# Kernel optimization log

Hardware: AMD Instinct MI355X
Metric: run time of the kernel (lower is better)

## Reference

```python
import jax, jax.numpy as jnp
import numpy as np

T, NNODES, DEG = 32, 10000, 32
IN_DIM, H1, HEADS, H2, GRU, PH = 128, 32, 4, 32, 32, 5


def setup_inputs() -> dict:
    key = jax.random.key(0)
    ks = jax.random.split(key, 24)
    d = {}
    d["h"] = jax.random.normal(ks[0], (T, NNODES, IN_DIM), jnp.float32)
    d["src"] = jax.random.randint(ks[1], (NNODES, DEG), 0, NNODES, dtype=jnp.int32)
    d["N"] = jnp.ones((1,), jnp.float32)
    d["I"] = jax.random.uniform(ks[2], (T,), jnp.float32)
    d["R"] = jax.random.uniform(ks[3], (T,), jnp.float32)
    d["S"] = jax.random.uniform(ks[4], (T,), jnp.float32)
    d["It"] = jax.random.uniform(ks[5], (T,), jnp.float32)
    d["Rt"] = jax.random.uniform(ks[6], (T,), jnp.float32)
    d["hx0"] = jax.random.normal(ks[7], (1, GRU), jnp.float32)
    # layer1: HEADS independent GATLayers (fc no-bias, attn_fc no-bias)
    d["W1"] = jax.random.normal(ks[8], (HEADS, IN_DIM, H1), jnp.float32) / np.sqrt(IN_DIM)
    d["a1"] = jax.random.normal(ks[9], (HEADS, 2 * H1), jnp.float32) / np.sqrt(2 * H1)
    # layer2: single head over concatenated features
    d["W2"] = jax.random.normal(ks[10], (1, HEADS * H1, H2), jnp.float32) / np.sqrt(HEADS * H1)
    d["a2"] = jax.random.normal(ks[11], (1, 2 * H2), jnp.float32) / np.sqrt(2 * H2)
    # GRUCell params (torch layout: W_ih [3*gru, in], W_hh [3*gru, gru])
    sg = 1.0 / np.sqrt(GRU)
    d["W_ih"] = jax.random.normal(ks[12], (3 * GRU, H2), jnp.float32) * sg
    d["W_hh"] = jax.random.normal(ks[13], (3 * GRU, GRU), jnp.float32) * sg
    d["b_ih"] = jax.random.normal(ks[14], (3 * GRU,), jnp.float32) * sg
    d["b_hh"] = jax.random.normal(ks[15], (3 * GRU,), jnp.float32) * sg
    sr = 1.0 / np.sqrt(GRU + 2)
    d["Wr1"] = jax.random.normal(ks[16], (2 * PH, GRU + 2), jnp.float32) * sr
    d["br1"] = jax.random.normal(ks[17], (2 * PH,), jnp.float32) * sr
    d["Wr2"] = jax.random.normal(ks[18], (2, GRU + 2), jnp.float32) * sr
    d["br2"] = jax.random.normal(ks[19], (2,), jnp.float32) * sr
    return d


def _gat(x, W, a, src):
    # x: [n, din]; W: [H, din, dout]; a: [H, 2*dout]; src: [n, D] in-neighbor ids
    dout = W.shape[-1]
    z = jnp.einsum('nd,hde->hne', x, W)                    # [H, n, dout]
    zs = z[:, src]                                          # [H, n, D, dout] mailbox of src feats
    e = (jnp.einsum('hnde,he->hnd', zs, a[:, :dout])        # a . z_src part
         + jnp.einsum('hne,he->hn', z, a[:, dout:])[:, :, None])  # a . z_dst part
    alpha = jax.nn.softmax(jax.nn.leaky_relu(e, 0.01), axis=-1)   # softmax over mailbox dim
    return jnp.einsum('hnd,hnde->hne', alpha, zs)           # [H, n, dout]


def reference(h, src, N, I, R, S, It, Rt, hx0, W1, a1, W2, a2,
              W_ih, W_hh, b_ih, b_hh, Wr1, br1, Wr2, br2):
    n = h.shape[1]
    Ns = N.squeeze()

    def step(hx, xs):
        iz, I_t, R_t, S_t, It_t, Rt_t = xs
        h1 = jax.nn.relu(_gat(iz, W1, a1, src))             # [H, n, H1]
        h1 = jnp.transpose(h1, (1, 0, 2)).reshape(n, -1)    # cat heads -> [n, H*H1]
        h2 = _gat(h1, W2, a2, src)[0]                       # [n, H2]
        cur = jnp.max(jax.nn.relu(h2), axis=0)[None, :]     # [1, H2]
        # GRUCell
        gi = cur @ W_ih.T + b_ih
        gh = hx @ W_hh.T + b_hh
        gir, giz, gin = jnp.split(gi, 3, axis=1)
        ghr, ghz, ghn = jnp.split(gh, 3, axis=1)
        r = jax.nn.sigmoid(gir + ghr)
        zg = jax.nn.sigmoid(giz + ghz)
        ng = jnp.tanh(gin + r * ghn)
        hx_new = (1.0 - zg) * ng + zg * hx                  # [1, GRU]
        new_hx = jnp.concatenate([hx_new, It_t.reshape(1, 1), Rt_t.reshape(1, 1)], axis=1)
        pred = (new_hx @ Wr1.T + br1).squeeze()             # [2*PH]
        ab = (new_hx @ Wr2.T + br2).squeeze()               # [2]
        a_s = jax.nn.sigmoid(ab[0])
        b_s = jax.nn.sigmoid(ab[1])
        new_I_t = pred[0::2]
        new_R_t = pred[1::2]
        # SIR physics rollout with detached recurrence
        last_I, last_R, last_S = I_t, R_t, S_t
        phyI, phyR = [], []
        dI = jnp.zeros(())
        dR = jnp.zeros(())
        for i in range(PH):
            if i > 0:
                last_I = last_I + jax.lax.stop_gradient(dI)
                last_R = last_R + jax.lax.stop_gradient(dR)
                last_S = Ns - last_I - last_R
            dI = a_s * last_I * (last_S / Ns) - b_s * last_I
            dR = b_s * last_I
            phyI.append(dI)
            phyR.append(dR)
        return hx_new, (new_I_t, new_R_t, jnp.stack(phyI), jnp.stack(phyR))

    _, (nI, nR, pI, pR) = jax.lax.scan(step, hx0, (h, I, R, S, It, Rt))
    return nI, nR, pI.reshape(-1), pR.reshape(-1)
```

## Files before the change

### kernel.cpp

```cpp
#include <hip/hip_runtime.h>

typedef __attribute__((ext_vector_type(8))) short short8;
typedef __attribute__((ext_vector_type(4))) float floatx4;
typedef __attribute__((ext_vector_type(2))) float float2v;
typedef __attribute__((ext_vector_type(4))) unsigned int uint4v;
typedef __attribute__((ext_vector_type(4))) int int4v;
typedef __attribute__((ext_vector_type(2))) unsigned int uint2v;

__device__ __forceinline__ float bf2f(unsigned short u) {
    return __uint_as_float(((unsigned int)u) << 16);
}
__device__ __forceinline__ unsigned short f2bf(float f) {
    unsigned int x = __float_as_uint(f);
    unsigned int r = (x + 0x7FFFu + ((x >> 16) & 1u)) >> 16;
    return (unsigned short)r;
}
__device__ __forceinline__ float ldf(const void* p, long i, bool f32) {
    return f32 ? ((const float*)p)[i] : bf2f(((const unsigned short*)p)[i]);
}
__device__ __forceinline__ bool detect_f32(const unsigned short* Nv) {
    return Nv[0] == 0;
}

#define P_WIH 0
#define P_WHH 3072
#define P_BIH 6144
#define P_BHH 6240
#define P_WR1 6336
#define P_BR1 6676
#define P_WR2 6686
#define P_BR2 6754
#define P_I   6756
#define P_R   6788
#define P_S   6820
#define P_IT  6852
#define P_RT  6884
#define P_N   6916
#define P_HX0 6917
#define P_TOT 6949

__global__ __launch_bounds__(256) void norm_params(
    const void* W1, const void* a1, const void* W2, const void* a2,
    const void* W_ih, const void* W_hh, const void* b_ih, const void* b_hh,
    const void* Wr1, const void* br1, const void* Wr2, const void* br2,
    const void* Iv, const void* Rv, const void* Sv, const void* Itv, const void* Rtv,
    const void* Nv, const void* hx0,
    float* __restrict__ P, unsigned short* __restrict__ WbT1,
    unsigned short* __restrict__ WbT2)
{
    bool f32 = detect_f32((const unsigned short*)Nv);
    int tid = threadIdx.x;
    struct Item { const void* p; int n; int off; };
    const Item items[15] = {
        {W_ih, 3072, P_WIH}, {W_hh, 3072, P_WHH}, {b_ih, 96, P_BIH}, {b_hh, 96, P_BHH},
        {Wr1, 340, P_WR1}, {br1, 10, P_BR1}, {Wr2, 68, P_WR2}, {br2, 2, P_BR2},
        {Iv, 32, P_I}, {Rv, 32, P_R}, {Sv, 32, P_S}, {Itv, 32, P_IT}, {Rtv, 32, P_RT},
        {Nv, 1, P_N}, {hx0, 32, P_HX0}
    };
    for (int it = 0; it < 15; it++)
        for (int i = tid; i < items[it].n; i += 256)
            P[items[it].off + i] = ldf(items[it].p, i, f32);

    for (int idx = tid; idx < 144 * 128; idx += 256) {
        int col = idx >> 7, k = idx & 127;
        float v = 0.f;
        if (col < 128) {
            int h = col >> 5, e = col & 31;
            v = ldf(W1, (h * 128 + k) * 32 + e, f32);
        } else if (col < 136) {
            int q = col - 128;
            int h = (q < 4) ? q : q - 4;
            int off = (q < 4) ? 0 : 32;
            float s = 0.f;
            for (int e = 0; e < 32; e++)
                s += ldf(W1, (h * 128 + k) * 32 + e, f32) * ldf(a1, h * 64 + off + e, f32);
            v = s;
        }
        WbT1[col * 128 + k] = f2bf(v);
    }
    for (int idx = tid; idx < 48 * 128; idx += 256) {
        int col = idx >> 7, k = idx & 127;
        float v = 0.f;
        if (col < 32) {
            v = ldf(W2, k * 32 + col, f32);
        } else if (col < 34) {
            int off = (col == 32) ? 0 : 32;
            float s = 0.f;
            for (int e = 0; e < 32; e++)
                s += ldf(W2, k * 32 + e, f32) * ldf(a2, off + e, f32);
            v = s;
        }
        WbT2[col * 128 + k] = f2bf(v);
    }
}

template<int NT, int HC, bool DYN>
__global__ __launch_bounds__(256) void gat_linear(
    const void* __restrict__ Xv, const unsigned short* __restrict__ WbT,
    unsigned short* __restrict__ Z, float* __restrict__ EL, float* __restrict__ ER,
    const unsigned short* __restrict__ Nv, long row0)
{
    constexpr int NCOL = NT * 16;
    constexpr int LDW  = 136;
    __shared__ unsigned short Ws[NCOL * LDW];
    int tid = threadIdx.x;
    for (int idx = tid; idx < NCOL * 16; idx += 256) {
        int col = idx >> 4, ch = idx & 15;
        *(uint4v*)(&Ws[col * LDW + ch * 8]) = *(const uint4v*)(&WbT[col * 128 + ch * 8]);
    }
    __syncthreads();

    bool f32 = DYN ? detect_f32(Nv) : false;
    int wave = tid >> 6, lane = tid & 63;
    int l15 = lane & 15, quad = lane >> 4;
    long lrow = (long)blockIdx.x * 64 + wave * 16;

    floatx4 acc[NT];
    floatx4 zz = {0.f, 0.f, 0.f, 0.f};
    #pragma unroll
    for (int i = 0; i < NT; i++) acc[i] = zz;

    long xoff = (row0 + lrow + l15) * 128 + quad * 8;
    #pragma unroll
    for (int kt = 0; kt < 4; kt++) {
        short8 afrag;
        if (DYN && f32) {
            const float* xr = (const float*)Xv + xoff + kt * 32;
            float4 u0 = ((const float4*)xr)[0];
            float4 u1 = ((const float4*)xr)[1];
            union { short8 v; unsigned short u[8]; } af;
            af.u[0] = f2bf(u0.x); af.u[1] = f2bf(u0.y);
            af.u[2] = f2bf(u0.z); af.u[3] = f2bf(u0.w);
            af.u[4] = f2bf(u1.x); af.u[5] = f2bf(u1.y);
            af.u[6] = f2bf(u1.z); af.u[7] = f2bf(u1.w);
            afrag = af.v;
        } else {
            afrag = *(const short8*)((const unsigned short*)Xv + xoff + kt * 32);
        }
        #pragma unroll
        for (int nt = 0; nt < NT; nt++) {
            short8 bfrag = *(const short8*)(&Ws[(nt * 16 + l15) * LDW + kt * 32 + quad * 8]);
            acc[nt] = __builtin_amdgcn_mfma_f32_16x16x32_bf16(afrag, bfrag, acc[nt], 0, 0, 0);
        }
    }

    #pragma unroll
    for (int nt = 0; nt < NT; nt++) {
        int col = nt * 16 + l15;
        #pragma unroll
        for (int r = 0; r < 4; r++) {
            long grow = lrow + quad * 4 + r;
            float v = acc[nt][r];
            if (col < HC * 32) {
                Z[grow * (HC * 32) + col] = f2bf(v);
            } else if (col < HC * 32 + HC) {
                EL[grow * HC + (col - HC * 32)] = v;
            } else if (col < HC * 32 + 2 * HC) {
                ER[grow * HC + (col - HC * 32 - HC)] = v;
            }
        }
    }
}

__global__ __launch_bounds__(256, 4) void gat1_aggr(
    const int* __restrict__ src,
    const unsigned short* __restrict__ Z,
    const float* __restrict__ EL,
    const float* __restrict__ ER,
    unsigned short* __restrict__ H1,
    int NX)
{
    __shared__ float als[4][4][33];
    int tid = threadIdx.x;
    int w = tid >> 6, lane = tid & 63;
    int d31 = lane & 31, g = lane >> 5;
    int fl = lane & 15, q = lane >> 4;
    int h = fl >> 2;

    int bid = blockIdx.x;
    int xcd = bid % NX;
    int j   = bid / NX;
    int tq  = j / 2500;
    int r   = j - tq * 2500;
    int t   = tq * NX + xcd;
    int tb  = t * 10000;
    int n   = r * 4 + w;
    int u   = tb + n;
    const char* Zb = (const char*)Z + (size_t)tb * 256;

    int sidx = src[n * 32 + d31];
    float2v el = *(const float2v*)(EL + (size_t)(tb + sidx) * 4 + g * 2);
    float2v er = *(const float2v*)(ER + (size_t)u * 4 + g * 2);
    float e0 = el[0] + er[0], e1 = el[1] + er[1];
    e0 = e0 >= 0.f ? e0 : 0.01f * e0;
    e1 = e1 >= 0.f ? e1 : 0.01f * e1;
    float m0 = e0, m1 = e1;
    #pragma unroll
    for (int off = 16; off > 0; off >>= 1) {
        m0 = fmaxf(m0, __shfl_xor(m0, off));
        m1 = fmaxf(m1, __shfl_xor(m1, off));
    }
    float x0 = __expf(e0 - m0), x1 = __expf(e1 - m1);
    float s0 = x0, s1 = x1;
    #pragma unroll
    for (int off = 16; off > 0; off >>= 1) {
        s0 += __shfl_xor(s0, off);
        s1 += __shfl_xor(s1, off);
    }
    als[w][2 * g + 0][d31] = x0 / s0;
    als[w][2 * g + 1][d31] = x1 / s1;
    __builtin_amdgcn_wave_barrier();

    const int* srow = src + n * 32 + q * 8;
    int4v mma = *(const int4v*)srow;
    int4v mmb = *(const int4v*)(srow + 4);

    uint4v ld[8];
    #pragma unroll
    for (int jj = 0; jj < 8; jj++) {
        int mm = (jj < 4) ? mma[jj & 3] : mmb[jj & 3];
        ld[jj] = *(const uint4v*)(Zb + (unsigned int)(mm * 256 + fl * 16));
    }
    float av[8];
    #pragma unroll
    for (int jj = 0; jj < 8; jj++)
        av[jj] = als[w][h][q * 8 + jj];

    float2v c[4];
    #pragma unroll
    for (int i = 0; i < 4; i++) c[i] = (float2v){0.f, 0.f};
    #pragma unroll
    for (int jj = 0; jj < 8; jj++) {
        float2v a2 = {av[jj], av[jj]};
        float2v f0 = {__uint_as_float(ld[jj].x << 16), __uint_as_float(ld[jj].x & 0xffff0000u)};
        float2v f1 = {__uint_as_float(ld[jj].y << 16), __uint_as_float(ld[jj].y & 0xffff0000u)};
        float2v f2 = {__uint_as_float(ld[jj].z << 16), __uint_as_float(ld[jj].z & 0xffff0000u)};
        float2v f3 = {__uint_as_float(ld[jj].w << 16), __uint_as_float(ld[jj].w & 0xffff0000u)};
        c[0] += a2 * f0;
        c[1] += a2 * f1;
        c[2] += a2 * f2;
        c[3] += a2 * f3;
    }
    #pragma unroll
    for (int i = 0; i < 4; i++) {
        c[i][0] += __shfl_xor(c[i][0], 16);
        c[i][1] += __shfl_xor(c[i][1], 16);
        c[i][0] += __shfl_xor(c[i][0], 32);
        c[i][1] += __shfl_xor(c[i][1], 32);
    }
    if (q == 0) {
        uint4v o;
        #pragma unroll
        for (int i = 0; i < 4; i++) {
            float lo = fmaxf(c[i][0], 0.f);
            float hi = fmaxf(c[i][1], 0.f);
            o[i] = (unsigned int)f2bf(lo) | ((unsigned int)f2bf(hi) << 16);
        }
        __builtin_nontemporal_store(o, (uint4v*)((char*)H1 + (size_t)u * 256 + fl * 16));
    }
}

__global__ __launch_bounds__(256, 4) void gat2_aggr(
    const int* __restrict__ src,
    const unsigned short* __restrict__ Z2,
    const float* __restrict__ EL2,
    const float* __restrict__ ER2,
    int* __restrict__ cur, int t0, int NX)
{
    __shared__ float als2[4][8][32];
    __shared__ int bm[32];
    int tid = threadIdx.x, w = tid >> 6, lane = tid & 63;
    int d31 = lane & 31, g = lane >> 5;
    int g3 = lane >> 3, f7 = lane & 7;

    int bid = blockIdx.x;
    int xcd = bid % NX;
    int j   = bid / NX;
    int tq  = j / 157;
    int r   = j - tq * 157;
    int t   = tq * NX + xcd;
    int tb  = t * 10000;
    int n0  = r * 64 + w * 16;
    const char* Zb = (const char*)Z2 + (size_t)tb * 64;

    if (tid < 32) bm[tid] = 0;
    __syncthreads();

    float m4[4] = {0.f, 0.f, 0.f, 0.f};
    #pragma unroll
    for (int b = 0; b < 2; b++) {
        int nb = n0 + b * 8;
        float ev[8];
        #pragma unroll
        for (int jj = 0; jj < 8; jj++) {
            int n = nb + jj;
            bool ok = n < 10000;
            int sidx = ok ? src[n * 32 + d31] : 0;
            float e = ok ? (EL2[tb + sidx] + ER2[tb + n]) : 0.f;
            ev[jj] = e >= 0.f ? e : 0.01f * e;
        }
        float mx[8];
        #pragma unroll
        for (int jj = 0; jj < 8; jj++) mx[jj] = ev[jj];
        #pragma unroll
        for (int off = 16; off > 0; off >>= 1) {
            #pragma unroll
            for (int jj = 0; jj < 8; jj++)
                mx[jj] = fmaxf(mx[jj], __shfl_xor(mx[jj], off));
        }
        float xv[8], sm[8];
        #pragma unroll
        for (int jj = 0; jj < 8; jj++) { xv[jj] = __expf(ev[jj] - mx[jj]); sm[jj] = xv[jj]; }
        #pragma unroll
        for (int off = 16; off > 0; off >>= 1) {
            #pragma unroll
            for (int jj = 0; jj < 8; jj++)
                sm[jj] += __shfl_xor(sm[jj], off);
        }
        if (g == 0) {
            #pragma unroll
            for (int jj = 0; jj < 8; jj++)
                als2[w][jj][d31] = xv[jj] / sm[jj];
        }
        __builtin_amdgcn_wave_barrier();

        #pragma unroll
        for (int jj = 0; jj < 8; jj++) {
            int n = nb + jj;
            if (n >= 10000) continue;
            floatx4 av4 = *(const floatx4*)&als2[w][jj][g3 * 4];
            int4v mv = *(const int4v*)(src + n * 32 + g3 * 4);
            uint2v ldv[4];
            #pragma unroll
            for (int k = 0; k < 4; k++)
                ldv[k] = *(const uint2v*)(Zb + (unsigned int)(mv[k] * 64 + f7 * 8));
            float c0 = 0.f, c1 = 0.f, c2 = 0.f, c3 = 0.f;
            #pragma unroll
            for (int k = 0; k < 4; k++) {
                c0 += av4[k] * __uint_as_float(ldv[k].x << 16);
                c1 += av4[k] * __uint_as_float(ldv[k].x & 0xffff0000u);
                c2 += av4[k] * __uint_as_float(ldv[k].y << 16);
                c3 += av4[k] * __uint_as_float(ldv[k].y & 0xffff0000u);
            }
            #pragma unroll
            for (int off = 8; off <= 32; off <<= 1) {
                c0 += __shfl_xor(c0, off);
                c1 += __shfl_xor(c1, off);
                c2 += __shfl_xor(c2, off);
                c3 += __shfl_xor(c3, off);
            }
            m4[0] = fmaxf(m4[0], c0);
            m4[1] = fmaxf(m4[1], c1);
            m4[2] = fmaxf(m4[2], c2);
            m4[3] = fmaxf(m4[3], c3);
        }
        __builtin_amdgcn_wave_barrier();
    }
    if (lane < 8) {
        #pragma unroll
        for (int i = 0; i < 4; i++)
            atomicMax(&bm[f7 * 4 + i], __float_as_int(m4[i]));
    }
    __syncthreads();
    if (tid < 32) atomicMax(&cur[(t0 + t) * 32 + tid], bm[tid]);
}

__global__ __launch_bounds__(128) void gru_head(
    const float* __restrict__ P, const float* __restrict__ cur,
    void* __restrict__ outv, const unsigned short* __restrict__ Nv)
{
    bool f32 = detect_f32(Nv);
    __shared__ float Whh[96 * 32], giAll[32 * 96];
    __shared__ float hx[32], gh[96], nh[34];
    int tid = threadIdx.x;
    for (int i = tid; i < 96 * 32; i += 128)
        Whh[i] = P[P_WHH + i];
    for (int o = tid; o < 32 * 96; o += 128) {
        int t = o / 96, gg = o - t * 96;
        float s = P[P_BIH + gg];
        for (int k = 0; k < 32; k++)
            s += cur[t * 32 + k] * P[P_WIH + gg * 32 + k];
        giAll[o] = s;
    }
    if (tid < 32) hx[tid] = P[P_HX0 + tid];
    __syncthreads();

    for (int t = 0; t < 32; t++) {
        if (tid < 96) {
            float sh = 0.f;
            for (int k = 0; k < 32; k++)
                sh += hx[k] * Whh[tid * 32 + k];
            gh[tid] = sh + P[P_BHH + tid];
        }
        __syncthreads();
        if (tid < 32) {
            const float* gi = &giAll[t * 96];
            float r  = 1.f / (1.f + __expf(-(gi[tid] + gh[tid])));
            float zg = 1.f / (1.f + __expf(-(gi[32 + tid] + gh[32 + tid])));
            float ng = tanhf(gi[64 + tid] + r * gh[64 + tid]);
            float hv = (1.f - zg) * ng + zg * hx[tid];
            hx[tid] = hv;
            nh[tid] = hv;
            if (tid == 0) { nh[32] = P[P_IT + t]; nh[33] = P[P_RT + t]; }
        }
        __syncthreads();
        if (tid < 10) {
            float s = P[P_BR1 + tid];
            for (int k = 0; k < 34; k++) s += nh[k] * P[P_WR1 + tid * 34 + k];
            int i = tid >> 1;
            int oi = ((tid & 1) == 0) ? (t * 5 + i) : (160 + t * 5 + i);
            if (f32) ((float*)outv)[oi] = s;
            else     ((unsigned short*)outv)[oi] = f2bf(s);
        }
        if (tid == 64) {
            float ab0 = P[P_BR2 + 0], ab1 = P[P_BR2 + 1];
            for (int k = 0; k < 34; k++) {
                ab0 += nh[k] * P[P_WR2 + k];
                ab1 += nh[k] * P[P_WR2 + 34 + k];
            }
            float a_s = 1.f / (1.f + __expf(-ab0));
            float b_s = 1.f / (1.f + __expf(-ab1));
            float Ns = P[P_N];
            float lI = P[P_I + t], lR = P[P_R + t], lS = P[P_S + t];
            float dI = 0.f, dR = 0.f;
            for (int i = 0; i < 5; i++) {
                if (i > 0) { lI += dI; lR += dR; lS = Ns - lI - lR; }
                dI = a_s * lI * (lS / Ns) - b_s * lI;
                dR = b_s * lI;
                if (f32) {
                    ((float*)outv)[320 + t * 5 + i] = dI;
                    ((float*)outv)[480 + t * 5 + i] = dR;
                } else {
                    ((unsigned short*)outv)[320 + t * 5 + i] = f2bf(dI);
                    ((unsigned short*)outv)[480 + t * 5 + i] = f2bf(dR);
                }
            }
        }
        __syncthreads();
    }
}

extern "C" void kernel_launch(void* const* d_in, const int* in_sizes, int n_in,
                              void* d_out, int out_size, void* d_ws, size_t ws_size,
                              hipStream_t stream) {
    const void* h    = d_in[0];
    const int*  src  = (const int*)d_in[1];
    const void* Nv   = d_in[2];
    const void* Iv   = d_in[3];
    const void* Rv   = d_in[4];
    const void* Sv   = d_in[5];
    const void* Itv  = d_in[6];
    const void* Rtv  = d_in[7];
    const void* hx0  = d_in[8];
    const void* W1   = d_in[9];
    const void* a1   = d_in[10];
    const void* W2   = d_in[11];
    const void* a2   = d_in[12];
    const void* W_ih = d_in[13];
    const void* W_hh = d_in[14];
    const void* b_ih = d_in[15];
    const void* b_hh = d_in[16];
    const void* Wr1  = d_in[17];
    const void* br1  = d_in[18];
    const void* Wr2  = d_in[19];
    const void* br2  = d_in[20];
    const unsigned short* Nu = (const unsigned short*)Nv;

    int TC = 4;
    for (int c = 32; c >= 4; c >>= 1) {
        size_t need = (size_t)c * 10000 * (128 * 2 + 128 * 2 + 16 + 16) + (1 << 20);
        if (need <= ws_size) { TC = c; break; }
    }
    long CR = (long)TC * 10000;

    char* ws = (char*)d_ws;
    size_t off = 0;
    auto alloc = [&](size_t b) {
        void* p = ws + off;
        off += (b + 255) & ~(size_t)255;
        return p;
    };
    float*          Pb   = (float*)alloc(P_TOT * 4);
    unsigned short* WbT1 = (unsigned short*)alloc(144 * 128 * 2);
    unsigned short* WbT2 = (unsigned short*)alloc(48 * 128 * 2);
    float*          cur  = (float*)alloc(32 * 32 * 4);
    unsigned short* z1   = (unsigned short*)alloc((size_t)CR * 128 * 2);
    unsigned short* h1   = (unsigned short*)alloc((size_t)CR * 128 * 2);
    float*          el1  = (float*)alloc((size_t)CR * 4 * 4);
    float*          er1  = (float*)alloc((size_t)CR * 4 * 4);
    unsigned short* z2   = z1;
    float*          el2  = el1;
    float*          er2  = er1;

    (void)hipMemsetAsync(cur, 0, 32 * 32 * 4, stream);
    norm_params<<<1, 256, 0, stream>>>(W1, a1, W2, a2, W_ih, W_hh, b_ih, b_hh,
                                       Wr1, br1, Wr2, br2, Iv, Rv, Sv, Itv, Rtv,
                                       Nv, hx0, Pb, WbT1, WbT2);
    int nchunks = 32 / TC;
    int g1 = (int)(CR / 64);
    int NX = TC < 8 ? TC : 8;
    int TQ = TC / NX;
    for (int c = 0; c < nchunks; c++) {
        long row0 = (long)c * CR;
        gat_linear<9, 4, true><<<g1, 256, 0, stream>>>(h, WbT1, z1, el1, er1, Nu, row0);
        gat1_aggr<<<NX * 2500 * TQ, 256, 0, stream>>>(src, z1, el1, er1, h1, NX);
        gat_linear<3, 1, false><<<g1, 256, 0, stream>>>(h1, WbT2, z2, el2, er2, Nu, 0);
        gat2_aggr<<<NX * 157 * TQ, 256, 0, stream>>>(src, z2, el2, er2, (int*)cur, c * TC, NX);
    }
    gru_head<<<1, 128, 0, stream>>>(Pb, cur, d_out, Nu);
}
```

Measured before the change: 714.8 us.

## Process eight nodes per wave in gat1_aggr with double-buffered gathers

Each wave in gat1_aggr now handles eight destination nodes instead of one. Attention softmax for all eight is computed up front, and the neighbor indices are staged in shared memory. The bf16 feature gathers for the next node are issued before the current node's weighted sum is computed, so gather latency overlaps with arithmetic. The grid shrinks by eight times and launch bounds drop to 3 waves per SIMD to make room for the larger register footprint, which trades occupancy for instruction-level parallelism.

```diff
diff --git a/kernel.cpp b/kernel.cpp
--- a/kernel.cpp
+++ b/kernel.cpp
@@ -162,7 +162,7 @@
     }
 }
 
-__global__ __launch_bounds__(256, 4) void gat1_aggr(
+__global__ __launch_bounds__(256, 3) void gat1_aggr(
     const int* __restrict__ src,
     const unsigned short* __restrict__ Z,
     const float* __restrict__ EL,
@@ -170,7 +170,8 @@
     unsigned short* __restrict__ H1,
     int NX)
 {
-    __shared__ float als[4][4][33];
+    __shared__ float als[4][8][4][36];
+    __shared__ int   sid[4][8][32];
     int tid = threadIdx.x;
     int w = tid >> 6, lane = tid & 63;
     int d31 = lane & 31, g = lane >> 5;
@@ -180,83 +181,129 @@
     int bid = blockIdx.x;
     int xcd = bid % NX;
     int j   = bid / NX;
-    int tq  = j / 2500;
-    int r   = j - tq * 2500;
+    int tq  = j / 313;
+    int r   = j - tq * 313;
     int t   = tq * NX + xcd;
     int tb  = t * 10000;
-    int n   = r * 4 + w;
-    int u   = tb + n;
+    int n0  = r * 32 + w * 8;
     const char* Zb = (const char*)Z + (size_t)tb * 256;
 
-    int sidx = src[n * 32 + d31];
-    float2v el = *(const float2v*)(EL + (size_t)(tb + sidx) * 4 + g * 2);
-    float2v er = *(const float2v*)(ER + (size_t)u * 4 + g * 2);
-    float e0 = el[0] + er[0], e1 = el[1] + er[1];
-    e0 = e0 >= 0.f ? e0 : 0.01f * e0;
-    e1 = e1 >= 0.f ? e1 : 0.01f * e1;
-    float m0 = e0, m1 = e1;
+    int sidx[8];
+    float2v elv[8], erv[8];
+    #pragma unroll
+    for (int jj = 0; jj < 8; jj++) {
+        int n = n0 + jj; n = n > 9999 ? 9999 : n;
+        sidx[jj] = src[n * 32 + d31];
+    }
+    #pragma unroll
+    for (int jj = 0; jj < 8; jj++)
+        elv[jj] = *(const float2v*)(EL + (size_t)(tb + sidx[jj]) * 4 + g * 2);
+    #pragma unroll
+    for (int jj = 0; jj < 8; jj++) {
+        int n = n0 + jj; n = n > 9999 ? 9999 : n;
+        erv[jj] = *(const float2v*)(ER + (size_t)(tb + n) * 4 + g * 2);
+    }
+    float e0[8], e1[8], m0[8], m1[8];
+    #pragma unroll
+    for (int jj = 0; jj < 8; jj++) {
+        float a = elv[jj][0] + erv[jj][0];
+        float b = elv[jj][1] + erv[jj][1];
+        e0[jj] = a >= 0.f ? a : 0.01f * a;
+        e1[jj] = b >= 0.f ? b : 0.01f * b;
+        m0[jj] = e0[jj]; m1[jj] = e1[jj];
+    }
     #pragma unroll
     for (int off = 16; off > 0; off >>= 1) {
-        m0 = fmaxf(m0, __shfl_xor(m0, off));
-        m1 = fmaxf(m1, __shfl_xor(m1, off));
-    }
-    float x0 = __expf(e0 - m0), x1 = __expf(e1 - m1);
-    float s0 = x0, s1 = x1;
+        #pragma unroll
+        for (int jj = 0; jj < 8; jj++) {
+            m0[jj] = fmaxf(m0[jj], __shfl_xor(m0[jj], off));
+            m1[jj] = fmaxf(m1[jj], __shfl_xor(m1[jj], off));
+        }
+    }
+    float x0[8], x1[8], s0[8], s1[8];
+    #pragma unroll
+    for (int jj = 0; jj < 8; jj++) {
+        x0[jj] = __expf(e0[jj] - m0[jj]);
+        x1[jj] = __expf(e1[jj] - m1[jj]);
+        s0[jj] = x0[jj]; s1[jj] = x1[jj];
+    }
     #pragma unroll
     for (int off = 16; off > 0; off >>= 1) {
-        s0 += __shfl_xor(s0, off);
-        s1 += __shfl_xor(s1, off);
-    }
-    als[w][2 * g + 0][d31] = x0 / s0;
-    als[w][2 * g + 1][d31] = x1 / s1;
+        #pragma unroll
+        for (int jj = 0; jj < 8; jj++) {
+            s0[jj] += __shfl_xor(s0[jj], off);
+            s1[jj] += __shfl_xor(s1[jj], off);
+        }
+    }
+    #pragma unroll
+    for (int jj = 0; jj < 8; jj++) {
+        als[w][jj][2 * g + 0][d31] = x0[jj] / s0[jj];
+        als[w][jj][2 * g + 1][d31] = x1[jj] / s1[jj];
+        if (g == 0) sid[w][jj][d31] = sidx[jj];
+    }
     __builtin_amdgcn_wave_barrier();
 
-    const int* srow = src + n * 32 + q * 8;
-    int4v mma = *(const int4v*)srow;
-    int4v mmb = *(const int4v*)(srow + 4);
-
-    uint4v ld[8];
+    uint4v buf[2][8];
+    {
+        int4v ia = *(const int4v*)&sid[w][0][q * 8];
+        int4v ib = *(const int4v*)&sid[w][0][q * 8 + 4];
+        #pragma unroll
+        for (int k = 0; k < 4; k++)
+            buf[0][k] = *(const uint4v*)(Zb + (unsigned int)(ia[k] * 256 + fl * 16));
+        #pragma unroll
+        for (int k = 0; k < 4; k++)
+            buf[0][4 + k] = *(const uint4v*)(Zb + (unsigned int)(ib[k] * 256 + fl * 16));
+    }
     #pragma unroll
     for (int jj = 0; jj < 8; jj++) {
-        int mm = (jj < 4) ? mma[jj & 3] : mmb[jj & 3];
-        ld[jj] = *(const uint4v*)(Zb + (unsigned int)(mm * 256 + fl * 16));
-    }
-    float av[8];
-    #pragma unroll
-    for (int jj = 0; jj < 8; jj++)
-        av[jj] = als[w][h][q * 8 + jj];
-
-    float2v c[4];
-    #pragma unroll
-    for (int i = 0; i < 4; i++) c[i] = (float2v){0.f, 0.f};
-    #pragma unroll
-    for (int jj = 0; jj < 8; jj++) {
-        float2v a2 = {av[jj], av[jj]};
-        float2v f0 = {__uint_as_float(ld[jj].x << 16), __uint_as_float(ld[jj].x & 0xffff0000u)};
-        float2v f1 = {__uint_as_float(ld[jj].y << 16), __uint_as_float(ld[jj].y & 0xffff0000u)};
-        float2v f2 = {__uint_as_float(ld[jj].z << 16), __uint_as_float(ld[jj].z & 0xffff0000u)};
-        float2v f3 = {__uint_as_float(ld[jj].w << 16), __uint_as_float(ld[jj].w & 0xffff0000u)};
-        c[0] += a2 * f0;
-        c[1] += a2 * f1;
-        c[2] += a2 * f2;
-        c[3] += a2 * f3;
-    }
-    #pragma unroll
-    for (int i = 0; i < 4; i++) {
-        c[i][0] += __shfl_xor(c[i][0], 16);
-        c[i][1] += __shfl_xor(c[i][1], 16);
-        c[i][0] += __shfl_xor(c[i][0], 32);
-        c[i][1] += __shfl_xor(c[i][1], 32);
-    }
-    if (q == 0) {
-        uint4v o;
+        int pb = jj & 1;
+        if (jj < 7) {
+            int4v ia = *(const int4v*)&sid[w][jj + 1][q * 8];
+            int4v ib = *(const int4v*)&sid[w][jj + 1][q * 8 + 4];
+            #pragma unroll
+            for (int k = 0; k < 4; k++)
+                buf[pb ^ 1][k] = *(const uint4v*)(Zb + (unsigned int)(ia[k] * 256 + fl * 16));
+            #pragma unroll
+            for (int k = 0; k < 4; k++)
+                buf[pb ^ 1][4 + k] = *(const uint4v*)(Zb + (unsigned int)(ib[k] * 256 + fl * 16));
+        }
+        floatx4 avA = *(const floatx4*)&als[w][jj][h][q * 8];
+        floatx4 avB = *(const floatx4*)&als[w][jj][h][q * 8 + 4];
+        float2v c[4];
+        #pragma unroll
+        for (int i = 0; i < 4; i++) c[i] = (float2v){0.f, 0.f};
+        #pragma unroll
+        for (int k = 0; k < 8; k++) {
+            float a = (k < 4) ? avA[k & 3] : avB[k & 3];
+            float2v a2 = {a, a};
+            uint4v ld = buf[pb][k];
+            float2v f0 = {__uint_as_float(ld.x << 16), __uint_as_float(ld.x & 0xffff0000u)};
+            float2v f1 = {__uint_as_float(ld.y << 16), __uint_as_float(ld.y & 0xffff0000u)};
+            float2v f2 = {__uint_as_float(ld.z << 16), __uint_as_float(ld.z & 0xffff0000u)};
+            float2v f3 = {__uint_as_float(ld.w << 16), __uint_as_float(ld.w & 0xffff0000u)};
+            c[0] += a2 * f0;
+            c[1] += a2 * f1;
+            c[2] += a2 * f2;
+            c[3] += a2 * f3;
+        }
         #pragma unroll
         for (int i = 0; i < 4; i++) {
-            float lo = fmaxf(c[i][0], 0.f);
-            float hi = fmaxf(c[i][1], 0.f);
-            o[i] = (unsigned int)f2bf(lo) | ((unsigned int)f2bf(hi) << 16);
-        }
-        __builtin_nontemporal_store(o, (uint4v*)((char*)H1 + (size_t)u * 256 + fl * 16));
+            c[i][0] += __shfl_xor(c[i][0], 16);
+            c[i][1] += __shfl_xor(c[i][1], 16);
+            c[i][0] += __shfl_xor(c[i][0], 32);
+            c[i][1] += __shfl_xor(c[i][1], 32);
+        }
+        if (q == 0 && n0 + jj < 10000) {
+            uint4v o;
+            #pragma unroll
+            for (int i = 0; i < 4; i++) {
+                float lo = fmaxf(c[i][0], 0.f);
+                float hi = fmaxf(c[i][1], 0.f);
+                o[i] = (unsigned int)f2bf(lo) | ((unsigned int)f2bf(hi) << 16);
+            }
+            __builtin_nontemporal_store(o,
+                (uint4v*)((char*)H1 + (size_t)(tb + n0 + jj) * 256 + fl * 16));
+        }
     }
 }
 
@@ -503,7 +550,7 @@
     for (int c = 0; c < nchunks; c++) {
         long row0 = (long)c * CR;
         gat_linear<9, 4, true><<<g1, 256, 0, stream>>>(h, WbT1, z1, el1, er1, Nu, row0);
-        gat1_aggr<<<NX * 2500 * TQ, 256, 0, stream>>>(src, z1, el1, er1, h1, NX);
+        gat1_aggr<<<NX * 313 * TQ, 256, 0, stream>>>(src, z1, el1, er1, h1, NX);
         gat_linear<3, 1, false><<<g1, 256, 0, stream>>>(h1, WbT2, z2, el2, er2, Nu, 0);
         gat2_aggr<<<NX * 157 * TQ, 256, 0, stream>>>(src, z2, el2, er2, (int*)cur, c * TC, NX);
     }
```

New measurement: 690.8 us. 3.4% less time.
